# Kernel tuning notes

Hardware: AMD Instinct MI355X
Metric: run time of the kernel (lower is better)

## Reference

```python
import jax, jax.numpy as jnp
import numpy as np

N, C, L, E = 10000, 128, 9, 5  # nodes, channels, (lmax+1)^2, num_elements
INV_SQRT_C = 1.0 / np.sqrt(C).astype(np.float32)


def _sparse(key, shape, p=0.15):
    # mimic the sparsity of e3nn CG coupling (U) tensors
    k1, k2 = jax.random.split(key)
    mask = jax.random.bernoulli(k1, p, shape)
    vals = jax.random.normal(k2, shape, dtype=jnp.float32)
    return jnp.where(mask, vals, 0.0)


def setup_inputs() -> dict:
    key = jax.random.key(0)
    ks = jax.random.split(key, 16)
    node_feats = jax.random.normal(ks[0], (N, C, L), dtype=jnp.float32)
    node_attrs = jax.nn.one_hot(jax.random.randint(ks[1], (N,), 0, E), E, dtype=jnp.float32)
    sc = jax.random.normal(ks[2], (N, 512), dtype=jnp.float32)
    # CG coupling tensors U_nu per output irrep (constant buffers in the torch module)
    # l_out = 0 (d=1): path counts k3=10, k2=3, k1=1
    U3_0 = _sparse(ks[3], (1, L, L, L, 10))
    U2_0 = _sparse(ks[4], (1, L, L, 3))
    U1_0 = _sparse(ks[5], (1, L, 1))
    # l_out = 1 (d=3): path counts k3=12, k2=4, k1=1
    U3_1 = _sparse(ks[6], (3, L, L, L, 12))
    U2_1 = _sparse(ks[7], (3, L, L, 4))
    U1_1 = _sparse(ks[8], (3, L, 1))
    # element-dependent contraction weights: randn(E, k, C) / k  (MACE init)
    w3_0 = jax.random.normal(ks[9], (E, 10, C), dtype=jnp.float32) / 10.0
    w2_0 = jax.random.normal(ks[10], (E, 3, C), dtype=jnp.float32) / 3.0
    w1_0 = jax.random.normal(ks[11], (E, 1, C), dtype=jnp.float32) / 1.0
    w3_1 = jax.random.normal(ks[12], (E, 12, C), dtype=jnp.float32) / 12.0
    w2_1 = jax.random.normal(ks[13], (E, 4, C), dtype=jnp.float32) / 4.0
    w1_1 = jax.random.normal(ks[14], (E, 1, C), dtype=jnp.float32) / 1.0
    # o3.Linear internal weights (one [C,C] block per output irrep)
    kl0, kl1 = jax.random.split(ks[15])
    lin_w0 = jax.random.normal(kl0, (C, C), dtype=jnp.float32)
    lin_w1 = jax.random.normal(kl1, (C, C), dtype=jnp.float32)
    return dict(node_feats=node_feats, node_attrs=node_attrs, sc=sc,
                U3_0=U3_0, U2_0=U2_0, U1_0=U1_0, w3_0=w3_0, w2_0=w2_0, w1_0=w1_0,
                U3_1=U3_1, U2_1=U2_1, U1_1=U1_1, w3_1=w3_1, w2_1=w2_1, w1_1=w1_1,
                lin_w0=lin_w0, lin_w1=lin_w1)


def _contraction(x, y, U3, U2, U1, w3, w2, w1):
    # MACE recursive symmetric contraction, correlation=3.
    # x: [N,C,L] node feats, y: [N,E] one-hot, U_nu: [d, L^nu, k_nu], w_nu: [E,k_nu,C]
    out = jnp.einsum('duvwk,ekc,bcw,be->bcduv', U3, w3, x, y)      # [N,C,d,L,L]
    c2 = jnp.einsum('duvk,ekc,be->bcduv', U2, w2, y) + out
    out = jnp.einsum('bcduv,bcv->bcdu', c2, x)                      # [N,C,d,L]
    c1 = jnp.einsum('duk,ekc,be->bcdu', U1, w1, y) + out
    out = jnp.einsum('bcdu,bcu->bcd', c1, x)                        # [N,C,d]
    return out.reshape(out.shape[0], -1)                            # [N,C*d]


def reference(node_feats, node_attrs, sc,
              U3_0, U2_0, U1_0, w3_0, w2_0, w1_0,
              U3_1, U2_1, U1_1, w3_1, w2_1, w1_1,
              lin_w0, lin_w1):
    # SymmetricContraction: one Contraction per target irrep, concat over irreps
    out0 = _contraction(node_feats, node_attrs, U3_0, U2_0, U1_0, w3_0, w2_0, w1_0)  # [N,C]
    out1 = _contraction(node_feats, node_attrs, U3_1, U2_1, U1_1, w3_1, w2_1, w1_1)  # [N,3C]
    # o3.Linear(target_irreps, target_irreps): per-l channel mixing, 1/sqrt(fan_in)
    y0 = (out0 @ lin_w0) * INV_SQRT_C                                # [N,C]
    x1 = out1.reshape(-1, C, 3)
    y1 = jnp.einsum('bcd,ce->bed', x1, lin_w1) * INV_SQRT_C          # [N,C,3]
    out = jnp.concatenate([y0, y1.reshape(-1, 3 * C)], axis=-1)      # [N,512]
    return out + sc  # use_sc residual
```

## Files before the change

kernel.cpp:

```cpp
#include <hip/hip_runtime.h>


#define CCH 128
#define LDIM 9
#define NE 5
#define BLK 256
#define TSTR 220
#define TGSTR 880
#define U3LDS 8748

__global__ __launch_bounds__(BLK) void count_offs_kernel(
    const float* __restrict__ attrs, int N,
    int* __restrict__ elem, int* __restrict__ gcnt,
    int* __restrict__ offs, int* __restrict__ cur) {
  int n = blockIdx.x * BLK + threadIdx.x;
  int e = 0;
  if (n < N) {
    const float* a = attrs + n * NE;
#pragma unroll
    for (int j = 1; j < NE; ++j)
      if (a[j] > 0.5f) e = j;
    elem[n] = e;
  }
  int lane = threadIdx.x & 63;
#pragma unroll
  for (int k = 0; k < NE; ++k) {
    unsigned long long m = __ballot(n < N && e == k);
    if (m) {
      int leader = __ffsll((long long)m) - 1;
      if (lane == leader) atomicAdd(&gcnt[k], __popcll(m));
    }
  }
  __threadfence();
  __syncthreads();
  if (threadIdx.x == 0) {
    int t = atomicAdd(&gcnt[NE], 1);
    if (t == (int)gridDim.x - 1) {
      int acc = 0;
      for (int k = 0; k < NE; ++k) {
        int ck = atomicAdd(&gcnt[k], 0);
        offs[k] = acc; cur[k] = acc; acc += ck;
      }
      offs[NE] = acc;
    }
  }
}

__global__ __launch_bounds__(BLK) void scatter_kernel(
    const int* __restrict__ elem, int N,
    int* __restrict__ cur, int* __restrict__ order) {
  int n = blockIdx.x * BLK + threadIdx.x;
  if (n >= N) return;
  int e = elem[n];
  int lane = threadIdx.x & 63;
#pragma unroll
  for (int k = 0; k < NE; ++k) {
    if (e == k) {
      unsigned long long m = __ballot(1);
      int cnt = __popcll(m);
      int leader = __ffsll((long long)m) - 1;
      int base = 0;
      if (lane == leader) base = atomicAdd(&cur[k], cnt);
      base = __shfl(base, leader);
      int rank = __popcll(m & ((1ull << lane) - 1ull));
      order[base + rank] = n;
    }
  }
}

__global__ __launch_bounds__(BLK) void table_kernel(
    const float* __restrict__ U3_0, const float* __restrict__ U2_0,
    const float* __restrict__ U1_0, const float* __restrict__ U3_1,
    const float* __restrict__ U2_1, const float* __restrict__ U1_1,
    const float* __restrict__ w3_0, const float* __restrict__ w2_0,
    const float* __restrict__ w1_0, const float* __restrict__ w3_1,
    const float* __restrict__ w2_1, const float* __restrict__ w1_1,
    float* __restrict__ table) {
  const int b = blockIdx.x;
  const int dd = blockIdx.y;
  const int e = b / CCH, c = b % CCH;
  float* Tg = table + (size_t)b * TGSTR + dd * TSTR;
  __shared__ float Us[U3LDS];
  __shared__ float U2s[324];
  __shared__ float R3[729];
  __shared__ float R2[81];
  __shared__ float R1l[9];
  __shared__ float w3l[12], w2l[4];
  const int tid = threadIdx.x;
  const int d = dd - 1;
  const int K3 = (dd == 0) ? 10 : 12;
  const int K2 = (dd == 0) ? 3 : 4;

  if (dd == 0) {
    for (int i = tid; i < 7290; i += BLK) Us[i] = U3_0[i];
    for (int i = tid; i < 243; i += BLK)  U2s[i] = U2_0[i];
    if (tid < 10) w3l[tid] = w3_0[(e * 10 + tid) * CCH + c];
    else if (tid < 13) w2l[tid - 10] = w2_0[(e * 3 + (tid - 10)) * CCH + c];
    if (tid < 9) R1l[tid] = U1_0[tid] * w1_0[e * CCH + c];
  } else {
    for (int i = tid; i < 8748; i += BLK) Us[i] = U3_1[d * 8748 + i];
    for (int i = tid; i < 324; i += BLK)  U2s[i] = U2_1[d * 324 + i];
    if (tid < 12) w3l[tid] = w3_1[(e * 12 + tid) * CCH + c];
    else if (tid < 16) w2l[tid - 12] = w2_1[(e * 4 + (tid - 12)) * CCH + c];
    if (tid < 9) R1l[tid] = U1_1[d * 9 + tid] * w1_1[e * CCH + c];
  }
  __syncthreads();
  for (int r = tid; r < 729; r += BLK) {
    float acc = 0.f;
    for (int k = 0; k < K3; ++k) acc += Us[r * K3 + k] * w3l[k];
    R3[r] = acc;
  }
  for (int q = tid; q < 81; q += BLK) {
    float acc = 0.f;
    for (int k = 0; k < K2; ++k) acc += U2s[q * K2 + k] * w2l[k];
    R2[q] = acc;
  }
  __syncthreads();
  for (int i = tid; i < TSTR; i += BLK) {
    float val = 0.f;
    if (i < 219) {
      int rem = i, u = 0;
      while (rem >= (10 - u) * (11 - u) / 2) {
        rem -= (10 - u) * (11 - u) / 2; ++u;
      }
      if (rem == 0) {
        val = R1l[u];
      } else {
        rem -= 1;
        int v = u;
        while (rem >= 10 - v) { rem -= 10 - v; ++v; }
        if (rem == 0) {
          val = (u == v) ? R2[u * 9 + v] : R2[u * 9 + v] + R2[v * 9 + u];
        } else {
          int w = v + (rem - 1);
          if (u == v && v == w)
            val = R3[(u * 9 + u) * 9 + u];
          else if (u == v)
            val = R3[(u * 9 + u) * 9 + w] + R3[(u * 9 + w) * 9 + u] +
                  R3[(w * 9 + u) * 9 + u];
          else if (v == w)
            val = R3[(u * 9 + v) * 9 + v] + R3[(v * 9 + u) * 9 + v] +
                  R3[(v * 9 + v) * 9 + u];
          else
            val = R3[(u * 9 + v) * 9 + w] + R3[(u * 9 + w) * 9 + v] +
                  R3[(v * 9 + u) * 9 + w] + R3[(v * 9 + w) * 9 + u] +
                  R3[(w * 9 + u) * 9 + v] + R3[(w * 9 + v) * 9 + u];
        }
      }
    }
    Tg[i] = val;
  }
}

__global__ __launch_bounds__(BLK, 8) void contract_kernel(
    const float* __restrict__ feats, const float* __restrict__ table,
    const int* __restrict__ order, const int* __restrict__ offs,
    float* __restrict__ tmp, int NPAD) {
  const int c = blockIdx.x;
  int rem = blockIdx.y;
  int e = -1, pbase = 0, segend = 0;
#pragma unroll
  for (int k = 0; k < NE; ++k) {
    int st = offs[k], en = offs[k + 1];
    int nc = (en - st + BLK - 1) >> 8;
    if (e < 0) {
      if (rem < nc) { e = k; pbase = st + rem * BLK; segend = en; }
      else rem -= nc;
    }
  }
  if (e < 0) return;

  const int p = pbase + threadIdx.x;
  const bool valid = (p < segend);
  const int n = order[valid ? p : (segend - 1)];

  float tf[LDIM];
  {
    const float* xp = feats + ((size_t)n * CCH + c) * LDIM;
#pragma unroll
    for (int q = 0; q < LDIM; ++q) tf[q] = xp[q];
  }

  const float* Tc = table + (size_t)(e * CCH + c) * TGSTR;

#pragma unroll 1
  for (int dd = 0; dd < 4; ++dd) {
    const float* B = Tc + dd * TSTR;
    int idx = 0;
    float acc = 0.f;
#pragma unroll
    for (int u = 0; u < 9; ++u) {
      float inner = B[idx++];
#pragma unroll
      for (int v = u; v < 9; ++v) {
        float Hv = B[idx++];
#pragma unroll
        for (int w = v; w < 9; ++w)
          Hv = fmaf(B[idx++], tf[w], Hv);
        inner = fmaf(Hv, tf[v], inner);
      }
      acc = fmaf(inner, tf[u], acc);
    }
    if (valid) tmp[((size_t)dd * CCH + c) * NPAD + p] = acc;
  }
}

__global__ __launch_bounds__(512, 8) void linear_kernel(
    const float* __restrict__ tmp, const float* __restrict__ W0,
    const float* __restrict__ W1, const float* __restrict__ sc,
    const int* __restrict__ order, float* __restrict__ out, int N, int NPAD) {
  const int nc = blockIdx.x >> 2, q = blockIdx.x & 3;
  const int p0 = nc * 64;
  const int t = threadIdx.x;
  const int lane = t & 63;
  const int dd = __builtin_amdgcn_readfirstlane((t >> 6) & 3);
  const int gl = __builtin_amdgcn_readfirstlane(t >> 8);
  const int c1b = q * 32 + gl * 16;
  const int p = p0 + lane;
  const int pc = (p < N) ? p : (N - 1);

  __shared__ float SROW[64 * 132];

  const float* Wm = (dd == 0) ? W0 : W1;
  const float* Ap = tmp + (size_t)dd * CCH * NPAD + pc;
  const float* Wb = Wm + c1b;

  float acc[16];
#pragma unroll
  for (int k = 0; k < 16; ++k) acc[k] = 0.f;

#pragma unroll 4
  for (int ci = 0; ci < CCH; ++ci) {
    const float a = Ap[(size_t)ci * NPAD];
    const float* wr = Wb + ci * CCH;
#pragma unroll
    for (int k = 0; k < 16; ++k)
      acc[k] = fmaf(a, wr[k], acc[k]);
  }

  const float s = 0.08838834764831843f;
  float* R = SROW + lane * 132;
  if (dd == 0) {
#pragma unroll
    for (int k = 0; k < 16; ++k) R[gl * 16 + k] = acc[k] * s;
  } else {
#pragma unroll
    for (int k = 0; k < 16; ++k)
      R[32 + (gl * 16 + k) * 3 + (dd - 1)] = acc[k] * s;
  }
  __syncthreads();

#pragma unroll
  for (int kk = 0; kk < 4; ++kk) {
    const int i = t + kk * 512;
    const int row = i >> 5, c4 = i & 31;
    const int pr = p0 + row;
    if (pr < N) {
      const int n = order[pr];
      const int gcol = (c4 < 8) ? (q * 32 + c4 * 4)
                                : (CCH + q * 96 + (c4 - 8) * 4);
      float4 v = *(const float4*)(SROW + row * 132 + c4 * 4);
      const float4 sv = *(const float4*)(sc + (size_t)n * 512 + gcol);
      v.x += sv.x; v.y += sv.y; v.z += sv.z; v.w += sv.w;
      *(float4*)(out + (size_t)n * 512 + gcol) = v;
    }
  }
}

extern "C" void kernel_launch(void* const* d_in, const int* in_sizes, int n_in,
                              void* d_out, int out_size, void* d_ws, size_t ws_size,
                              hipStream_t stream) {
  const float* feats = (const float*)d_in[0];
  const float* attrs = (const float*)d_in[1];
  const float* sc    = (const float*)d_in[2];
  const float* U3_0  = (const float*)d_in[3];
  const float* U2_0  = (const float*)d_in[4];
  const float* U1_0  = (const float*)d_in[5];
  const float* w3_0  = (const float*)d_in[6];
  const float* w2_0  = (const float*)d_in[7];
  const float* w1_0  = (const float*)d_in[8];
  const float* U3_1  = (const float*)d_in[9];
  const float* U2_1  = (const float*)d_in[10];
  const float* U1_1  = (const float*)d_in[11];
  const float* w3_1  = (const float*)d_in[12];
  const float* w2_1  = (const float*)d_in[13];
  const float* w1_1  = (const float*)d_in[14];
  const float* W0    = (const float*)d_in[15];
  const float* W1    = (const float*)d_in[16];

  const int N = in_sizes[0] / (CCH * LDIM);
  const int NPAD = ((N + 15) & ~15) + 16;

  float* table = (float*)d_ws;
  float* tmp   = table + (size_t)NE * CCH * TGSTR;
  int*   order = (int*)(tmp + (size_t)4 * CCH * NPAD);
  int*   elem  = order + N;
  int*   offs  = elem + N;
  int*   cur   = offs + 8;
  int*   gcnt  = cur + 8;
  float* out   = (float*)d_out;

  hipMemsetAsync(gcnt, 0, 8 * sizeof(int), stream);

  const int nblk = (N + BLK - 1) / BLK;
  count_offs_kernel<<<dim3(nblk), dim3(BLK), 0, stream>>>(
      attrs, N, elem, gcnt, offs, cur);
  scatter_kernel<<<dim3(nblk), dim3(BLK), 0, stream>>>(elem, N, cur, order);

  table_kernel<<<dim3(NE * CCH, 4), dim3(BLK), 0, stream>>>(
      U3_0, U2_0, U1_0, U3_1, U2_1, U1_1,
      w3_0, w2_0, w1_0, w3_1, w2_1, w1_1, table);

  const int chunksMax = (N + BLK - 1) / BLK + NE;
  contract_kernel<<<dim3(CCH, chunksMax), dim3(BLK), 0, stream>>>(
      feats, table, order, offs, tmp, NPAD);

  const int lgrid = ((N + 63) / 64) * 4;
  linear_kernel<<<dim3(lgrid), dim3(512), 0, stream>>>(
      tmp, W0, W1, sc, order, out, N, NPAD);
}
```

Baseline: 257.8 us.

## Split linear stage into separate l=0 and l=1 kernels with 256-node tiles

Replaces the combined linear kernel with two kernels: one for the scalar irrep and one for the vector irrep. Each block covers 256 nodes and 16 output channels, with the d component on the z grid dimension. This raises node-level parallelism per block and simplifies indexing. In exchange, each tmp row is reread across more column blocks, and the l=1 outputs are written as strided scalars rather than float4, which may hurt coalescing.

Result: no change. 260.4 us (+1.0%).

```diff
diff --git a/kernel.cpp b/kernel.cpp
--- a/kernel.cpp
+++ b/kernel.cpp
@@ -205,25 +205,19 @@
   }
 }
 
-__global__ __launch_bounds__(512, 8) void linear_kernel(
+__global__ __launch_bounds__(BLK, 8) void linear0_kernel(
     const float* __restrict__ tmp, const float* __restrict__ W0,
-    const float* __restrict__ W1, const float* __restrict__ sc,
-    const int* __restrict__ order, float* __restrict__ out, int N, int NPAD) {
-  const int nc = blockIdx.x >> 2, q = blockIdx.x & 3;
-  const int p0 = nc * 64;
+    const float* __restrict__ sc, const int* __restrict__ order,
+    float* __restrict__ out, int N, int NPAD) {
   const int t = threadIdx.x;
-  const int lane = t & 63;
-  const int dd = __builtin_amdgcn_readfirstlane((t >> 6) & 3);
-  const int gl = __builtin_amdgcn_readfirstlane(t >> 8);
-  const int c1b = q * 32 + gl * 16;
-  const int p = p0 + lane;
+  const int p = blockIdx.x * BLK + t;
+  const int c1b = blockIdx.y * 16;
   const int pc = (p < N) ? p : (N - 1);
 
-  __shared__ float SROW[64 * 132];
-
-  const float* Wm = (dd == 0) ? W0 : W1;
-  const float* Ap = tmp + (size_t)dd * CCH * NPAD + pc;
-  const float* Wb = Wm + c1b;
+  __shared__ float SR[BLK * 20];
+
+  const float* Ap = tmp + pc;
+  const float* Wb = W0 + c1b;
 
   float acc[16];
 #pragma unroll
@@ -239,30 +233,74 @@
   }
 
   const float s = 0.08838834764831843f;
-  float* R = SROW + lane * 132;
-  if (dd == 0) {
-#pragma unroll
-    for (int k = 0; k < 16; ++k) R[gl * 16 + k] = acc[k] * s;
-  } else {
-#pragma unroll
-    for (int k = 0; k < 16; ++k)
-      R[32 + (gl * 16 + k) * 3 + (dd - 1)] = acc[k] * s;
-  }
-  __syncthreads();
-
-#pragma unroll
-  for (int kk = 0; kk < 4; ++kk) {
-    const int i = t + kk * 512;
-    const int row = i >> 5, c4 = i & 31;
-    const int pr = p0 + row;
-    if (pr < N) {
-      const int n = order[pr];
-      const int gcol = (c4 < 8) ? (q * 32 + c4 * 4)
-                                : (CCH + q * 96 + (c4 - 8) * 4);
-      float4 v = *(const float4*)(SROW + row * 132 + c4 * 4);
+#pragma unroll
+  for (int k = 0; k < 16; ++k) SR[t * 20 + k] = acc[k] * s;
+  __syncthreads();
+
+#pragma unroll
+  for (int k = 0; k < 4; ++k) {
+    const int idx = t + k * BLK;
+    const int node = idx >> 2, f = idx & 3;
+    const int p2 = blockIdx.x * BLK + node;
+    if (p2 < N) {
+      const int n = order[p2];
+      const int gcol = c1b + f * 4;
+      float4 v;
+      v.x = SR[node * 20 + f * 4 + 0];
+      v.y = SR[node * 20 + f * 4 + 1];
+      v.z = SR[node * 20 + f * 4 + 2];
+      v.w = SR[node * 20 + f * 4 + 3];
       const float4 sv = *(const float4*)(sc + (size_t)n * 512 + gcol);
       v.x += sv.x; v.y += sv.y; v.z += sv.z; v.w += sv.w;
       *(float4*)(out + (size_t)n * 512 + gcol) = v;
+    }
+  }
+}
+
+__global__ __launch_bounds__(BLK, 8) void linear1_kernel(
+    const float* __restrict__ tmp, const float* __restrict__ W1,
+    const float* __restrict__ sc, const int* __restrict__ order,
+    float* __restrict__ out, int N, int NPAD) {
+  const int t = threadIdx.x;
+  const int p = blockIdx.x * BLK + t;
+  const int c1b = blockIdx.y * 16;
+  const int dd = blockIdx.z + 1;
+  const int pc = (p < N) ? p : (N - 1);
+
+  __shared__ float SR[BLK * 20];
+
+  const float* Ap = tmp + (size_t)dd * CCH * NPAD + pc;
+  const float* Wb = W1 + c1b;
+
+  float acc[16];
+#pragma unroll
+  for (int k = 0; k < 16; ++k) acc[k] = 0.f;
+
+#pragma unroll 4
+  for (int ci = 0; ci < CCH; ++ci) {
+    const float a = Ap[(size_t)ci * NPAD];
+    const float* wr = Wb + ci * CCH;
+#pragma unroll
+    for (int k = 0; k < 16; ++k)
+      acc[k] = fmaf(a, wr[k], acc[k]);
+  }
+
+  const float s = 0.08838834764831843f;
+#pragma unroll
+  for (int k = 0; k < 16; ++k) SR[t * 20 + k] = acc[k] * s;
+  __syncthreads();
+
+  const int jj = t & 15;
+  const int nb0 = t >> 4;
+#pragma unroll 1
+  for (int nb = 0; nb < 16; ++nb) {
+    const int node = nb0 + nb * 16;
+    const int p2 = blockIdx.x * BLK + node;
+    if (p2 < N) {
+      const int n = order[p2];
+      const int gcol = CCH + 3 * (c1b + jj) + (dd - 1);
+      const float v = SR[node * 20 + jj];
+      out[(size_t)n * 512 + gcol] = v + sc[(size_t)n * 512 + gcol];
     }
   }
 }
@@ -315,7 +353,9 @@
   contract_kernel<<<dim3(CCH, chunksMax), dim3(BLK), 0, stream>>>(
       feats, table, order, offs, tmp, NPAD);
 
-  const int lgrid = ((N + 63) / 64) * 4;
-  linear_kernel<<<dim3(lgrid), dim3(512), 0, stream>>>(
-      tmp, W0, W1, sc, order, out, N, NPAD);
-}
+  const int nchunk = (N + BLK - 1) / BLK;
+  linear1_kernel<<<dim3(nchunk, 8, 3), dim3(BLK), 0, stream>>>(
+      tmp, W1, sc, order, out, N, NPAD);
+  linear0_kernel<<<dim3(nchunk, 8), dim3(BLK), 0, stream>>>(
+      tmp, W0, sc, order, out, N, NPAD);
+}
```
